# Performance work log

Measured on AMD Instinct MI355X. Metric: run time of the kernel, lower is better.

Reference implementation:

```python
import jax, jax.numpy as jnp
import numpy as np

B, S, D, H = 2, 2048, 1024, 16
DK = D // H

def setup_inputs() -> dict:
    key = jax.random.key(0)
    ks = jax.random.split(key, 12)
    scale = 1.0 / np.sqrt(D)
    inp = {
        'q': jax.random.normal(ks[0], (B, S, D), jnp.float32),
        'k': jax.random.normal(ks[1], (B, S, D), jnp.float32),
        'v': jax.random.normal(ks[2], (B, S, D), jnp.float32),
        # causal mask: 1 where attending is allowed (j <= i), 0 for future tokens
        'mask': jnp.tril(jnp.ones((S, S), jnp.int32))[None, None, :, :],
        'wq': jax.random.normal(ks[3], (D, D), jnp.float32) * scale,
        'bq': jnp.zeros((D,), jnp.float32),
        'wk': jax.random.normal(ks[4], (D, D), jnp.float32) * scale,
        'bk': jnp.zeros((D,), jnp.float32),
        'wv': jax.random.normal(ks[5], (D, D), jnp.float32) * scale,
        'bv': jnp.zeros((D,), jnp.float32),
        'wo': jax.random.normal(ks[6], (D, D), jnp.float32) * scale,
        'bo': jnp.zeros((D,), jnp.float32),
    }
    return inp


def reference(q, k, v, mask, wq, bq, wk, bk, wv, bv, wo, bo):
    def split_heads(x):
        # [B,S,D] -> [B,H,S,DK]
        return x.reshape(B, S, H, DK).transpose(0, 2, 1, 3)

    query = split_heads(q @ wq + bq)
    key_ = split_heads(k @ wk + bk)
    value = split_heads(v @ wv + bv)

    # [B,H,S,S] attention scores
    scores = jnp.einsum('bhqd,bhkd->bhqk', query, key_) / jnp.sqrt(
        jnp.asarray(DK, jnp.float32))
    scores = jnp.where(mask == 0, jnp.asarray(-1e9, scores.dtype), scores)
    attn = jax.nn.softmax(scores, axis=-1)  # dropout p=0.0 (eval mode)

    x = jnp.einsum('bhqk,bhkd->bhqd', attn, value)  # [B,H,S,DK]
    x = x.transpose(0, 2, 1, 3).reshape(B, S, D)
    return x @ wo + bo
```

## Files before the change

### kernel.cpp

```cpp
#include <hip/hip_runtime.h>
#include <hip/hip_bf16.h>

#define BATCH 2
#define SEQ   2048
#define DMODEL 1024
#define NHEAD 16
#define DK    64
#define MTOK  (BATCH * SEQ)

typedef __attribute__((ext_vector_type(8))) short bf16x8;
typedef __attribute__((ext_vector_type(4))) float f32x4;

__device__ __forceinline__ unsigned short f2bf(float x) {
    unsigned u = __float_as_uint(x);
    u = (u + 0x7FFFu + ((u >> 16) & 1u)) >> 16;
    return (unsigned short)u;
}

__device__ __forceinline__ void store_out(float* p, float v)          { *p = v; }
__device__ __forceinline__ void store_out(unsigned short* p, float v) { *p = f2bf(v); }

__device__ __forceinline__ void g2lds16(const void* g, void* l) {
    __builtin_amdgcn_global_load_lds(
        (const __attribute__((address_space(1))) void*)g,
        (__attribute__((address_space(3))) void*)l, 16, 0, 0);
}

__global__ __launch_bounds__(256) void cvt3_bf16_kernel(
    const float* __restrict__ s0, const float* __restrict__ s1,
    const float* __restrict__ s2,
    unsigned short* __restrict__ d0, unsigned short* __restrict__ d1,
    unsigned short* __restrict__ d2, int n)
{
    const float* src; unsigned short* dst;
    switch (blockIdx.z) {
        case 0:  src = s0; dst = d0; break;
        case 1:  src = s1; dst = d1; break;
        default: src = s2; dst = d2; break;
    }
    int i = (blockIdx.x * 256 + threadIdx.x) * 8;
    if (i >= n) return;
    float4 a = *(const float4*)(src + i);
    float4 b = *(const float4*)(src + i + 4);
    union { unsigned short s[8]; uint4 u; } o;
    o.s[0] = f2bf(a.x); o.s[1] = f2bf(a.y); o.s[2] = f2bf(a.z); o.s[3] = f2bf(a.w);
    o.s[4] = f2bf(b.x); o.s[5] = f2bf(b.y); o.s[6] = f2bf(b.z); o.s[7] = f2bf(b.w);
    *(uint4*)(dst + i) = o.u;
}

__global__ __launch_bounds__(256) void wtrans_kernel(
    const float* __restrict__ w0, const float* __restrict__ w1,
    const float* __restrict__ w2, const float* __restrict__ w3,
    unsigned short* __restrict__ t0, unsigned short* __restrict__ t1,
    unsigned short* __restrict__ t2, unsigned short* __restrict__ t3)
{
    __shared__ float tile[32][33];
    const float* W; unsigned short* T;
    switch (blockIdx.z) {
        case 0:  W = w0; T = t0; break;
        case 1:  W = w1; T = t1; break;
        case 2:  W = w2; T = t2; break;
        default: W = w3; T = t3; break;
    }
    const int n0 = blockIdx.x * 32, k0 = blockIdx.y * 32;
    const int t  = threadIdx.x;
    const int r  = t >> 3;
    const int c4 = (t & 7) * 4;

    float4 v = *(const float4*)&W[(size_t)(k0 + r) * DMODEL + n0 + c4];
    tile[r][c4 + 0] = v.x; tile[r][c4 + 1] = v.y;
    tile[r][c4 + 2] = v.z; tile[r][c4 + 3] = v.w;
    __syncthreads();

    union { unsigned short s[4]; uint2 u; } o;
#pragma unroll
    for (int u = 0; u < 4; ++u) o.s[u] = f2bf(tile[c4 + u][r]);
    *(uint2*)&T[(size_t)(n0 + r) * DMODEL + k0 + c4] = o.u;
}

struct GemmP {
    const unsigned short* A;
    const unsigned short* Bt;
    const float* bias;
    void* C;
    int N, K, ctShift, biasByRow;
    float scale;
};
struct Gemm3 { GemmP p[3]; };

template <typename OutT, int NTILE>
__global__ __launch_bounds__(256) void gemm_lds_kernel(Gemm3 g)
{
    __shared__ unsigned short sA[16 * 512];
    __shared__ unsigned short sB[4 * NTILE * 512];

    const GemmP p = g.p[blockIdx.z];
    const unsigned short* __restrict__ A  = p.A;
    const unsigned short* __restrict__ Bt = p.Bt;
    OutT* __restrict__ C = (OutT*)p.C;
    const int K = p.K, N = p.N;

    const int bid = blockIdx.x;
    const int bx = bid & ((1 << p.ctShift) - 1);
    const int by = bid >> p.ctShift;
    const int row0 = by * 128;
    const int col0 = bx * (NTILE * 32);

    const int t    = threadIdx.x;
    const int w    = t >> 6;
    const int lane = t & 63;
    const int ln   = lane & 15;
    const int qg   = lane >> 4;
    const int wm   = w >> 1;
    const int wn   = w & 1;

    const int PW = 4 + NTILE;
    const unsigned short* sp[PW];
    unsigned short* lp[PW];
#pragma unroll
    for (int i = 0; i < PW; ++i) {
        const int s = w * PW + i;
        if (s < 16) {
            const int mtg = s >> 1, kc = s & 1;
            sp[i] = A + (size_t)(row0 + mtg * 16 + ln) * K + kc * 32 + qg * 8;
            lp[i] = &sA[s * 512];
        } else {
            const int bi = s - 16;
            const int ntg = bi >> 1, kc = bi & 1;
            sp[i] = Bt + (size_t)(col0 + ntg * 16 + ln) * K + kc * 32 + qg * 8;
            lp[i] = &sB[bi * 512];
        }
    }

    f32x4 acc[4][NTILE];
#pragma unroll
    for (int mt = 0; mt < 4; ++mt)
#pragma unroll
        for (int nt = 0; nt < NTILE; ++nt) acc[mt][nt] = (f32x4){0.f, 0.f, 0.f, 0.f};

    for (int kt = 0; kt < K / 64; ++kt) {
        __syncthreads();
        const int koff = kt * 64;
#pragma unroll
        for (int i = 0; i < PW; ++i)
            g2lds16(sp[i] + koff, lp[i]);
        __syncthreads();

#pragma unroll
        for (int kc = 0; kc < 2; ++kc) {
            bf16x8 aF[4], bF[NTILE];
#pragma unroll
            for (int mt = 0; mt < 4; ++mt)
                aF[mt] = *(const bf16x8*)&sA[(((wm * 4 + mt) * 2) + kc) * 512 + lane * 8];
#pragma unroll
            for (int nt = 0; nt < NTILE; ++nt)
                bF[nt] = *(const bf16x8*)&sB[(((wn * NTILE + nt) * 2) + kc) * 512 + lane * 8];
#pragma unroll
            for (int mt = 0; mt < 4; ++mt)
#pragma unroll
                for (int nt = 0; nt < NTILE; ++nt)
                    acc[mt][nt] = __builtin_amdgcn_mfma_f32_16x16x32_bf16(
                        aF[mt], bF[nt], acc[mt][nt], 0, 0, 0);
        }
    }

    float bcol[NTILE], brow[4][4];
    if (!p.biasByRow) {
#pragma unroll
        for (int nt = 0; nt < NTILE; ++nt)
            bcol[nt] = p.bias[col0 + wn * NTILE * 16 + nt * 16 + ln];
    } else {
#pragma unroll
        for (int mt = 0; mt < 4; ++mt)
#pragma unroll
            for (int r = 0; r < 4; ++r)
                brow[mt][r] = p.bias[row0 + wm * 64 + mt * 16 + qg * 4 + r];
    }

#pragma unroll
    for (int mt = 0; mt < 4; ++mt)
#pragma unroll
        for (int nt = 0; nt < NTILE; ++nt)
#pragma unroll
            for (int r = 0; r < 4; ++r) {
                int row = row0 + wm * 64 + mt * 16 + qg * 4 + r;
                int col = col0 + wn * NTILE * 16 + nt * 16 + ln;
                float bb = p.biasByRow ? brow[mt][r] : bcol[nt];
                store_out(&C[(size_t)row * N + col], (acc[mt][nt][r] + bb) * p.scale);
            }
}

#define BR 64
#define BC 64
#define PSTR 72

__global__ __launch_bounds__(256) void attn_mfma_kernel(
    const unsigned short* __restrict__ Qg, const unsigned short* __restrict__ Kg,
    const unsigned short* __restrict__ VT, unsigned short* __restrict__ O)
{
    __shared__ unsigned short sK[2][8 * 512];
    __shared__ unsigned short sV[2][8 * 512];
    __shared__ unsigned short sQ[8 * 512];
    __shared__ unsigned short sP[BR * PSTR];

    const int t    = threadIdx.x;
    const int w    = t >> 6;
    const int lane = t & 63;
    const int ln   = lane & 15;
    const int qg   = lane >> 4;

    const int id  = blockIdx.x;
    const int bh  = id & 31;
    const int qt  = (SEQ / BR - 1) - (id >> 5);
    const int b   = bh >> 4;
    const int h   = bh & 15;
    const int qi0 = qt * BR;

    const size_t rowbase = (size_t)b * SEQ;
    const size_t colbase = (size_t)h * DK;

#pragma unroll
    for (int i = 0; i < 2; ++i) {
        const int s = w * 2 + i;
        const int nt = s >> 1, kc = s & 1;
        g2lds16(Qg + (rowbase + qi0 + w * 16 + ln) * DMODEL + colbase + i * 32 + qg * 8,
                &sQ[s * 512]);
        g2lds16(Kg + (rowbase + nt * 16 + ln) * DMODEL + colbase + kc * 32 + qg * 8,
                &sK[0][s * 512]);
        g2lds16(VT + (size_t)(colbase + nt * 16 + ln) * MTOK + rowbase + kc * 32 + qg * 8,
                &sV[0][s * 512]);
    }
    __syncthreads();

    bf16x8 aq[2];
#pragma unroll
    for (int kc = 0; kc < 2; ++kc)
        aq[kc] = *(const bf16x8*)&sQ[(w * 2 + kc) * 512 + lane * 8];

    const short one_bf = (short)0x3F80;
    const bf16x8 bone = (bf16x8){one_bf, one_bf, one_bf, one_bf,
                                 one_bf, one_bf, one_bf, one_bf};

    f32x4 ofrag[4];
#pragma unroll
    for (int nt = 0; nt < 4; ++nt) ofrag[nt] = (f32x4){0.f, 0.f, 0.f, 0.f};
    f32x4 osum = (f32x4){0.f, 0.f, 0.f, 0.f};
    float m_r[4];
#pragma unroll
    for (int r = 0; r < 4; ++r) m_r[r] = -3.0e38f;

    const int ntiles = qt + 1;
    for (int jt = 0; jt < ntiles; ++jt) {
        const int cur = jt & 1;

        if (jt + 1 < ntiles) {
            const int j1 = (jt + 1) * BC;
            const int nb = cur ^ 1;
#pragma unroll
            for (int i = 0; i < 2; ++i) {
                const int s = w * 2 + i;
                const int nt = s >> 1, kc = s & 1;
                g2lds16(Kg + (rowbase + j1 + nt * 16 + ln) * DMODEL + colbase + kc * 32 + qg * 8,
                        &sK[nb][s * 512]);
                g2lds16(VT + (size_t)(colbase + nt * 16 + ln) * MTOK + rowbase + j1 + kc * 32 + qg * 8,
                        &sV[nb][s * 512]);
            }
        }

        f32x4 sf[4];
#pragma unroll
        for (int nt = 0; nt < 4; ++nt) {
            f32x4 a2 = (f32x4){0.f, 0.f, 0.f, 0.f};
#pragma unroll
            for (int kc = 0; kc < 2; ++kc) {
                bf16x8 bk = *(const bf16x8*)&sK[cur][(nt * 2 + kc) * 512 + lane * 8];
                a2 = __builtin_amdgcn_mfma_f32_16x16x32_bf16(aq[kc], bk, a2, 0, 0, 0);
            }
            sf[nt] = a2;
        }

        if (jt == ntiles - 1) {
#pragma unroll
            for (int nt = 0; nt < 4; ++nt)
#pragma unroll
                for (int r = 0; r < 4; ++r) {
                    int qrow = w * 16 + qg * 4 + r;
                    int col  = nt * 16 + ln;
                    if (col > qrow) sf[nt][r] = -1.0e30f;
                }
        }

        float rmax[4];
#pragma unroll
        for (int r = 0; r < 4; ++r)
            rmax[r] = fmaxf(fmaxf(sf[0][r], sf[1][r]), fmaxf(sf[2][r], sf[3][r]));
#pragma unroll
        for (int off = 8; off >= 1; off >>= 1)
#pragma unroll
            for (int r = 0; r < 4; ++r)
                rmax[r] = fmaxf(rmax[r], __shfl_xor(rmax[r], off));

        float alpha[4];
#pragma unroll
        for (int r = 0; r < 4; ++r) {
            float mn = fmaxf(m_r[r], rmax[r]);
            alpha[r] = exp2f(m_r[r] - mn);
            m_r[r] = mn;
        }

#pragma unroll
        for (int nt = 0; nt < 4; ++nt)
#pragma unroll
            for (int r = 0; r < 4; ++r) {
                float pv = exp2f(sf[nt][r] - m_r[r]);
                int row = w * 16 + qg * 4 + r;
                int col = (nt * 16 + ln) ^ (((w * 4 + qg) & 7) * 8);
                sP[row * PSTR + col] = f2bf(pv);
            }

#pragma unroll
        for (int nt = 0; nt < 4; ++nt)
#pragma unroll
            for (int r = 0; r < 4; ++r) ofrag[nt][r] *= alpha[r];
#pragma unroll
        for (int r = 0; r < 4; ++r) osum[r] *= alpha[r];

        bf16x8 apf[2];
#pragma unroll
        for (int kc = 0; kc < 2; ++kc) {
            int row = w * 16 + ln;
            int col = (kc * 32 + qg * 8) ^ ((((row >> 2) & 7)) * 8);
            apf[kc] = *(const bf16x8*)&sP[row * PSTR + col];
        }

#pragma unroll
        for (int kc = 0; kc < 2; ++kc)
            osum = __builtin_amdgcn_mfma_f32_16x16x32_bf16(apf[kc], bone, osum, 0, 0, 0);
#pragma unroll
        for (int nt = 0; nt < 4; ++nt) {
#pragma unroll
            for (int kc = 0; kc < 2; ++kc) {
                bf16x8 bv = *(const bf16x8*)&sV[cur][(nt * 2 + kc) * 512 + lane * 8];
                ofrag[nt] = __builtin_amdgcn_mfma_f32_16x16x32_bf16(apf[kc], bv, ofrag[nt], 0, 0, 0);
            }
        }

        __syncthreads();
    }

    float inv[4];
#pragma unroll
    for (int r = 0; r < 4; ++r) inv[r] = 1.0f / osum[r];
#pragma unroll
    for (int nt = 0; nt < 4; ++nt)
#pragma unroll
        for (int r = 0; r < 4; ++r) {
            int gq = qi0 + w * 16 + qg * 4 + r;
            O[(rowbase + gq) * DMODEL + colbase + nt * 16 + ln] =
                f2bf(ofrag[nt][r] * inv[r]);
        }
}

extern "C" void kernel_launch(void* const* d_in, const int* in_sizes, int n_in,
                              void* d_out, int out_size, void* d_ws, size_t ws_size,
                              hipStream_t stream)
{
    const float* q  = (const float*)d_in[0];
    const float* k  = (const float*)d_in[1];
    const float* v  = (const float*)d_in[2];
    const float* wq = (const float*)d_in[4];
    const float* bq = (const float*)d_in[5];
    const float* wk = (const float*)d_in[6];
    const float* bk = (const float*)d_in[7];
    const float* wv = (const float*)d_in[8];
    const float* bv = (const float*)d_in[9];
    const float* wo = (const float*)d_in[10];
    const float* bo = (const float*)d_in[11];
    float* out = (float*)d_out;

    const size_t mat  = (size_t)MTOK * DMODEL;
    const size_t wmat = (size_t)DMODEL * DMODEL;
    unsigned short* Abq = (unsigned short*)d_ws;
    unsigned short* Abk = Abq + mat;
    unsigned short* Abv = Abk + mat;
    unsigned short* WtQ = Abv + mat;
    unsigned short* WtK = WtQ + wmat;
    unsigned short* WtV = WtK + wmat;
    unsigned short* WtO = WtV + wmat;
    unsigned short* Qb  = WtO + wmat;
    unsigned short* Kb  = Qb + mat;
    unsigned short* VT  = Kb + mat;
    unsigned short* CTX = VT + mat;

    cvt3_bf16_kernel<<<dim3((unsigned)(mat / 2048), 1, 3), 256, 0, stream>>>(
        q, k, v, Abq, Abk, Abv, (int)mat);
    wtrans_kernel<<<dim3(32, 32, 4), 256, 0, stream>>>(wq, wk, wv, wo, WtQ, WtK, WtV, WtO);

    const float qscale = 0.125f * 1.44269504088896f;
    Gemm3 g;
    g.p[0] = (GemmP){Abq, WtQ, bq, (void*)Qb, DMODEL, DMODEL, 3, 0, qscale};
    g.p[1] = (GemmP){Abk, WtK, bk, (void*)Kb, DMODEL, DMODEL, 3, 0, 1.0f};
    g.p[2] = (GemmP){WtV, Abv, bv, (void*)VT, MTOK,   DMODEL, 5, 1, 1.0f};
    gemm_lds_kernel<unsigned short, 4><<<dim3(256, 1, 3), 256, 0, stream>>>(g);

    attn_mfma_kernel<<<BATCH * NHEAD * (SEQ / BR), 256, 0, stream>>>(Qb, Kb, VT, CTX);

    Gemm3 go;
    go.p[0] = (GemmP){CTX, WtO, bo, (void*)out, DMODEL, DMODEL, 4, 0, 1.0f};
    go.p[1] = go.p[0];
    go.p[2] = go.p[0];
    gemm_lds_kernel<float, 2><<<dim3(512, 1, 1), 256, 0, stream>>>(go);
}
```

Before: 273.2 us.

## Double-buffer GEMM LDS tiles with explicit vmcnt waits to overlap loads

Reworks the bf16 GEMM main loop to use two LDS buffers, prefetching tiles two K-steps ahead through global_load_lds. Explicit s_waitcnt vmcnt and s_barrier calls replace the two __syncthreads per iteration. The aim is to hide global-load latency behind the MFMA work. The cost is double the LDS footprint per block, which may lower occupancy, plus hand-written wait counts that rely on PW loads being in flight per wave.

New measurement: 258.6 us. 5.3% less time.

```diff
diff --git a/kernel.cpp b/kernel.cpp
--- a/kernel.cpp
+++ b/kernel.cpp
@@ -24,6 +24,17 @@
     __builtin_amdgcn_global_load_lds(
         (const __attribute__((address_space(1))) void*)g,
         (__attribute__((address_space(3))) void*)l, 16, 0, 0);
+}
+
+template <int N>
+__device__ __forceinline__ void s_wait_vmcnt() {
+    asm volatile("s_waitcnt vmcnt(%0)" :: "n"(N) : "memory");
+}
+__device__ __forceinline__ void s_wait_lgkm0() {
+    asm volatile("s_waitcnt lgkmcnt(0)" ::: "memory");
+}
+__device__ __forceinline__ void s_bar() {
+    asm volatile("s_barrier" ::: "memory");
 }
 
 __global__ __launch_bounds__(256) void cvt3_bf16_kernel(
@@ -91,8 +102,11 @@
 template <typename OutT, int NTILE>
 __global__ __launch_bounds__(256) void gemm_lds_kernel(Gemm3 g)
 {
-    __shared__ unsigned short sA[16 * 512];
-    __shared__ unsigned short sB[4 * NTILE * 512];
+    constexpr int NBLK  = 16 + 4 * NTILE;
+    constexpr int BUFSZ = NBLK * 512;
+    constexpr int PW    = NBLK / 4;
+
+    __shared__ unsigned short sS[2][BUFSZ];
 
     const GemmP p = g.p[blockIdx.z];
     const unsigned short* __restrict__ A  = p.A;
@@ -114,7 +128,6 @@
     const int wm   = w >> 1;
     const int wn   = w & 1;
 
-    const int PW = 4 + NTILE;
     const unsigned short* sp[PW];
     unsigned short* lp[PW];
 #pragma unroll
@@ -123,13 +136,12 @@
         if (s < 16) {
             const int mtg = s >> 1, kc = s & 1;
             sp[i] = A + (size_t)(row0 + mtg * 16 + ln) * K + kc * 32 + qg * 8;
-            lp[i] = &sA[s * 512];
         } else {
             const int bi = s - 16;
             const int ntg = bi >> 1, kc = bi & 1;
             sp[i] = Bt + (size_t)(col0 + ntg * 16 + ln) * K + kc * 32 + qg * 8;
-            lp[i] = &sB[bi * 512];
-        }
+        }
+        lp[i] = &sS[0][s * 512];
     }
 
     f32x4 acc[4][NTILE];
@@ -138,37 +150,57 @@
 #pragma unroll
         for (int nt = 0; nt < NTILE; ++nt) acc[mt][nt] = (f32x4){0.f, 0.f, 0.f, 0.f};
 
-    for (int kt = 0; kt < K / 64; ++kt) {
-        __syncthreads();
-        const int koff = kt * 64;
-#pragma unroll
-        for (int i = 0; i < PW; ++i)
-            g2lds16(sp[i] + koff, lp[i]);
-        __syncthreads();
-
+    const int nt = K / 64;
+
+#pragma unroll
+    for (int i = 0; i < PW; ++i) g2lds16(sp[i], lp[i]);
+    if (nt > 1) {
+#pragma unroll
+        for (int i = 0; i < PW; ++i) g2lds16(sp[i] + 64, lp[i] + BUFSZ);
+    }
+
+    int cur = 0;
+    for (int kt = 0; kt < nt; ++kt) {
+        if (kt < nt - 1) s_wait_vmcnt<PW>();
+        else             s_wait_vmcnt<0>();
+        s_bar();
+
+        const unsigned short* bufA = &sS[cur][0];
+        const unsigned short* bufB = &sS[cur][16 * 512];
 #pragma unroll
         for (int kc = 0; kc < 2; ++kc) {
             bf16x8 aF[4], bF[NTILE];
 #pragma unroll
             for (int mt = 0; mt < 4; ++mt)
-                aF[mt] = *(const bf16x8*)&sA[(((wm * 4 + mt) * 2) + kc) * 512 + lane * 8];
-#pragma unroll
-            for (int nt = 0; nt < NTILE; ++nt)
-                bF[nt] = *(const bf16x8*)&sB[(((wn * NTILE + nt) * 2) + kc) * 512 + lane * 8];
+                aF[mt] = *(const bf16x8*)&bufA[(((wm * 4 + mt) * 2) + kc) * 512 + lane * 8];
+#pragma unroll
+            for (int n2 = 0; n2 < NTILE; ++n2)
+                bF[n2] = *(const bf16x8*)&bufB[(((wn * NTILE + n2) * 2) + kc) * 512 + lane * 8];
 #pragma unroll
             for (int mt = 0; mt < 4; ++mt)
 #pragma unroll
-                for (int nt = 0; nt < NTILE; ++nt)
-                    acc[mt][nt] = __builtin_amdgcn_mfma_f32_16x16x32_bf16(
-                        aF[mt], bF[nt], acc[mt][nt], 0, 0, 0);
-        }
+                for (int n2 = 0; n2 < NTILE; ++n2)
+                    acc[mt][n2] = __builtin_amdgcn_mfma_f32_16x16x32_bf16(
+                        aF[mt], bF[n2], acc[mt][n2], 0, 0, 0);
+        }
+
+        s_wait_lgkm0();
+        s_bar();
+
+        if (kt + 2 < nt) {
+            const int koff = (kt + 2) * 64;
+#pragma unroll
+            for (int i = 0; i < PW; ++i)
+                g2lds16(sp[i] + koff, lp[i] + cur * BUFSZ);
+        }
+        cur ^= 1;
     }
 
     float bcol[NTILE], brow[4][4];
     if (!p.biasByRow) {
 #pragma unroll
-        for (int nt = 0; nt < NTILE; ++nt)
-            bcol[nt] = p.bias[col0 + wn * NTILE * 16 + nt * 16 + ln];
+        for (int n2 = 0; n2 < NTILE; ++n2)
+            bcol[n2] = p.bias[col0 + wn * NTILE * 16 + n2 * 16 + ln];
     } else {
 #pragma unroll
         for (int mt = 0; mt < 4; ++mt)
@@ -180,13 +212,13 @@
 #pragma unroll
     for (int mt = 0; mt < 4; ++mt)
 #pragma unroll
-        for (int nt = 0; nt < NTILE; ++nt)
+        for (int n2 = 0; n2 < NTILE; ++n2)
 #pragma unroll
             for (int r = 0; r < 4; ++r) {
                 int row = row0 + wm * 64 + mt * 16 + qg * 4 + r;
-                int col = col0 + wn * NTILE * 16 + nt * 16 + ln;
-                float bb = p.biasByRow ? brow[mt][r] : bcol[nt];
-                store_out(&C[(size_t)row * N + col], (acc[mt][nt][r] + bb) * p.scale);
+                int col = col0 + wn * NTILE * 16 + n2 * 16 + ln;
+                float bb = p.biasByRow ? brow[mt][r] : bcol[n2];
+                store_out(&C[(size_t)row * N + col], (acc[mt][n2][r] + bb) * p.scale);
             }
 }
 
```
